# Optimization experiments

Measured on AMD Instinct MI355X. Metric: run time of the kernel, lower is better.

## Reference

```python
import jax, jax.numpy as jnp
import numpy as np

W, BHS, SEQ, H = 8, 2, 1024, 2048
FFN_PER = (4 * H) // W  # per-partition 4h width = 1024

def setup_inputs() -> dict:
    key = jax.random.key(0)
    k1, k2, k3 = jax.random.split(key, 3)
    # xavier-normal-ish scale for weights
    s1 = (2.0 / (H + FFN_PER)) ** 0.5
    s2 = (2.0 / (FFN_PER + H)) ** 0.5
    return {
        "hidden_states": jax.random.normal(k1, (W, BHS, SEQ, H), dtype=jnp.float32),
        "w1": jax.random.normal(k2, (W, H, FFN_PER), dtype=jnp.float32) * s1,
        "b1": jnp.zeros((W, 1, FFN_PER), dtype=jnp.float32),
        "w2": jax.random.normal(k3, (W, FFN_PER, H), dtype=jnp.float32) * s2,
        "b2": jnp.zeros((W, H), dtype=jnp.float32),
        "idx_list": jnp.arange(W, dtype=jnp.int64),
    }

def reference(hidden_states, w1, b1, w2, b2, idx_list):
    w, bhs, seq, h = hidden_states.shape
    # view [W, bhs, seq, h] -> [W, bhs*seq, h]
    x = hidden_states.reshape(w, bhs * seq, h)
    # column-parallel: baddbmm(bias, x, w1) -> [W, N, 4h/W]
    inter = jnp.einsum('wnh,whf->wnf', x, w1) + b1
    # exact (erf) gelu, matching torch F.gelu default
    inter = jax.nn.gelu(inter, approximate=False)
    # row-parallel: baddbmm(bias, inter, w2) -> [W, N, h]
    out_bias = b2[:, None, :]  # [W, 1, out]
    out = jnp.einsum('wnf,wfo->wno', inter, w2) + out_bias
    return (out, out_bias)
```

## Files before the change

kernel.cpp:

```cpp
#include <hip/hip_runtime.h>
#include <hip/hip_bf16.h>
#include <math.h>


typedef float f32x4 __attribute__((ext_vector_type(4)));
typedef short bf16x8 __attribute__((ext_vector_type(8)));
typedef short bf16x4 __attribute__((ext_vector_type(4)));
typedef unsigned short u16;

#define NW 8
#define MDIM 2048
#define HDIM 2048
#define FFN  1024

static __device__ __forceinline__ u16 f32_to_bf16_rn(float f) {
  union { float f; unsigned u; } v; v.f = f;
  unsigned r = v.u + 0x7FFF + ((v.u >> 16) & 1);
  return (u16)(r >> 16);
}

static __device__ __forceinline__ void gload_lds16(const void* g, void* l) {
  __builtin_amdgcn_global_load_lds(
      (const __attribute__((address_space(1))) void*)g,
      (__attribute__((address_space(3))) void*)l, 16, 0, 0);
}

__global__ void convert_bf16_kernel(const float* __restrict__ in,
                                    u16* __restrict__ out) {
  size_t i = (size_t)blockIdx.x * blockDim.x + threadIdx.x;
  f32x4 v = ((const f32x4*)in)[i];
  bf16x4 p;
  p[0] = (short)f32_to_bf16_rn(v.x);
  p[1] = (short)f32_to_bf16_rn(v.y);
  p[2] = (short)f32_to_bf16_rn(v.z);
  p[3] = (short)f32_to_bf16_rn(v.w);
  ((bf16x4*)out)[i] = p;
}

__global__ void convert_transpose_kernel(const float* __restrict__ in,
                                         u16* __restrict__ out, int R, int C) {
  __shared__ u16 tile[64][68];
  int w = blockIdx.z;
  int c0 = blockIdx.x * 64, r0 = blockIdx.y * 64;
  int t = threadIdx.x;
  const float* ip = in + (size_t)w * R * C;
  u16* op = out + (size_t)w * C * R;
  int tr = t >> 4;
  int tc4 = (t & 15) * 4;
#pragma unroll
  for (int j = 0; j < 4; ++j) {
    int r = tr + j * 16;
    f32x4 v = *(const f32x4*)(ip + (size_t)(r0 + r) * C + c0 + tc4);
    tile[r][tc4 + 0] = f32_to_bf16_rn(v.x);
    tile[r][tc4 + 1] = f32_to_bf16_rn(v.y);
    tile[r][tc4 + 2] = f32_to_bf16_rn(v.z);
    tile[r][tc4 + 3] = f32_to_bf16_rn(v.w);
  }
  __syncthreads();
#pragma unroll
  for (int j = 0; j < 4; ++j) {
    int c = tr + j * 16;
    bf16x4 p;
    p[0] = (short)tile[tc4 + 0][c];
    p[1] = (short)tile[tc4 + 1][c];
    p[2] = (short)tile[tc4 + 2][c];
    p[3] = (short)tile[tc4 + 3][c];
    *(bf16x4*)(op + (size_t)(c0 + c) * R + r0 + tc4) = p;
  }
}

#define STAGE_AH(dst, tt, h)                                                  \
  do {                                                                        \
    gload_lds16(gA + (size_t)(h) * 128 * rowK + (size_t)(tt) * 128,           \
                (dst) + (h) * 16384 + tid * 16);                              \
    gload_lds16(gA + ((size_t)(h) * 128 + 64) * rowK + (size_t)(tt) * 128,    \
                (dst) + (h) * 16384 + 8192 + tid * 16);                       \
  } while (0)
#define STAGE_BH(dst, tt, h)                                                  \
  do {                                                                        \
    gload_lds16(gB + (size_t)(h) * 128 * rowK + (size_t)(tt) * 128,           \
                (dst) + 32768 + (h) * 16384 + tid * 16);                      \
    gload_lds16(gB + ((size_t)(h) * 128 + 64) * rowK + (size_t)(tt) * 128,    \
                (dst) + 32768 + (h) * 16384 + 8192 + tid * 16);               \
  } while (0)

#define DO_PHASE(SB, q, first, STAGES, VMCODE)                                \
  {                                                                           \
    if (first) {                                                              \
      _Pragma("unroll") for (int jj = 0; jj < 4; ++jj)                        \
          _Pragma("unroll") for (int kk = 0; kk < 2; ++kk)                    \
              bfr[jj][kk] = *(const bf16x8*)((SB) + Boff +                    \
                  (brow + jj * 16 + ra) * 128 + (colsw ^ (kk << 6)));         \
    }                                                                         \
    _Pragma("unroll") for (int ii = 0; ii < 2; ++ii)                          \
        _Pragma("unroll") for (int kk = 0; kk < 2; ++kk)                      \
            afr[ii][kk] = *(const bf16x8*)((SB) + Aoff +                      \
                ((q)*32 + ii * 16 + ra) * 128 + (colsw ^ (kk << 6)));         \
    STAGES;                                                                   \
    __builtin_amdgcn_s_barrier();                                             \
    asm volatile("s_waitcnt lgkmcnt(0)" ::: "memory");                        \
    __builtin_amdgcn_sched_barrier(0);                                        \
    __builtin_amdgcn_s_setprio(1);                                            \
    _Pragma("unroll") for (int ii = 0; ii < 2; ++ii)                          \
        _Pragma("unroll") for (int jj = 0; jj < 4; ++jj)                      \
            _Pragma("unroll") for (int kk = 0; kk < 2; ++kk)                  \
                acc[(q)*2 + ii][jj] =                                         \
                    __builtin_amdgcn_mfma_f32_16x16x32_bf16(                  \
                        afr[ii][kk], bfr[jj][kk], acc[(q)*2 + ii][jj],        \
                        0, 0, 0);                                             \
    __builtin_amdgcn_s_setprio(0);                                            \
    VMCODE;                                                                   \
    __builtin_amdgcn_s_barrier();                                             \
  }

template <bool GELU, bool C_F32>
__global__ __launch_bounds__(512, 2) void mlp_gemm(
    const u16* __restrict__ A, const u16* __restrict__ Bt,
    const float* __restrict__ bias, void* __restrict__ Cptr,
    int M, int N, int K, int nN) {
  __shared__ __align__(16) char lds[131072];
  char* cur = lds;
  char* nxt = lds + 65536;

  const int bid = blockIdx.x;
  const int w = bid & 7;
  const int jb = bid >> 3;
  const int m0 = (jb / nN) * 256;
  const int n0 = (jb % nN) * 256;

  const int tid = threadIdx.x;
  const int wid = tid >> 6, lane = tid & 63;
  const int wr = wid >> 2, wc = wid & 3;
  const int qa = lane >> 4, ra = lane & 15;

  const u16* ap = A + (size_t)w * M * K;
  const u16* btp = Bt + (size_t)w * N * K;
  const float* bp = bias + (size_t)w * N;

  const size_t rowK = (size_t)K * 2;
  const int r8 = tid >> 3;
  const int csw = ((tid & 7) * 16) ^ ((r8 & 7) << 4);
  const char* gA = (const char*)ap + (size_t)(m0 + r8) * rowK + csw;
  const char* gB = (const char*)btp + (size_t)(n0 + r8) * rowK + csw;

  const int colsw = (qa * 16) ^ ((ra & 7) << 4);
  const int Aoff = wr * 16384;
  const int Boff = 32768 + (wc >> 1) * 16384;
  const int brow = (wc & 1) * 64;

  f32x4 acc[8][4];
#pragma unroll
  for (int i = 0; i < 8; ++i)
#pragma unroll
    for (int j = 0; j < 4; ++j)
#pragma unroll
      for (int r = 0; r < 4; ++r) acc[i][j][r] = 0.0f;

  const int NT = K >> 6;
  const int nIter = NT >> 1;

  STAGE_BH(cur, 0, 0); STAGE_BH(cur, 0, 1);
  STAGE_AH(cur, 0, 0); STAGE_AH(cur, 0, 1);
  STAGE_BH(nxt, 1, 0); STAGE_BH(nxt, 1, 1);
  asm volatile("s_waitcnt vmcnt(4)" ::: "memory");
  __builtin_amdgcn_sched_barrier(0);
  __builtin_amdgcn_s_barrier();

  bf16x8 bfr[4][2], afr[2][2];
  for (int it = 0; it < nIter; ++it) {
    const int t = it * 2;
    const bool s2 = (t + 2) < NT, s3 = (t + 3) < NT;

    DO_PHASE(cur, 0, 1, { STAGE_AH(nxt, t + 1, 0); }, {});
    DO_PHASE(cur, 1, 0,
             { STAGE_AH(nxt, t + 1, 1); if (s2) STAGE_BH(cur, t + 2, 0); }, {});
    DO_PHASE(cur, 2, 0, { if (s2) STAGE_BH(cur, t + 2, 1); }, {});
    DO_PHASE(cur, 3, 0, {}, {
      if (s2) asm volatile("s_waitcnt vmcnt(4)" ::: "memory");
      else    asm volatile("s_waitcnt vmcnt(0)" ::: "memory");
      __builtin_amdgcn_sched_barrier(0);
    });
    DO_PHASE(nxt, 0, 1, { if (s2) STAGE_AH(cur, t + 2, 0); }, {});
    DO_PHASE(nxt, 1, 0,
             { if (s2) STAGE_AH(cur, t + 2, 1); if (s3) STAGE_BH(nxt, t + 3, 0); }, {});
    DO_PHASE(nxt, 2, 0, { if (s3) STAGE_BH(nxt, t + 3, 1); }, {});
    DO_PHASE(nxt, 3, 0, {}, {
      if (s3) asm volatile("s_waitcnt vmcnt(4)" ::: "memory");
      else    asm volatile("s_waitcnt vmcnt(0)" ::: "memory");
      __builtin_amdgcn_sched_barrier(0);
    });
  }

#pragma unroll
  for (int i = 0; i < 8; ++i) {
#pragma unroll
    for (int j = 0; j < 4; ++j) {
      int col = n0 + wc * 64 + j * 16 + ra;
      float bv = bp[col];
#pragma unroll
      for (int r = 0; r < 4; ++r) {
        int row = m0 + wr * 128 + i * 16 + qa * 4 + r;
        float v = acc[i][j][r] + bv;
        if (GELU) v = 0.5f * v * (1.0f + erff(v * 0.70710678118654752f));
        if (C_F32)
          ((float*)Cptr)[(size_t)w * M * N + (size_t)row * N + col] = v;
        else
          ((u16*)Cptr)[(size_t)w * M * N + (size_t)row * N + col] =
              f32_to_bf16_rn(v);
      }
    }
  }
}

__global__ void bias_out_kernel(const float* __restrict__ b2,
                                float* __restrict__ outb) {
  int i = blockIdx.x * 256 + threadIdx.x;
  if (i < NW * HDIM) outb[i] = b2[i];
}

extern "C" void kernel_launch(void* const* d_in, const int* in_sizes, int n_in,
                              void* d_out, int out_size, void* d_ws,
                              size_t ws_size, hipStream_t stream) {
  const float* hs = (const float*)d_in[0];
  const float* w1 = (const float*)d_in[1];
  const float* b1 = (const float*)d_in[2];
  const float* w2 = (const float*)d_in[3];
  const float* b2 = (const float*)d_in[4];

  u16* W1t = (u16*)d_ws;
  u16* W2t = W1t + (size_t)NW * FFN * HDIM;
  u16* inter = W2t + (size_t)NW * HDIM * FFN;
  u16* XbWs = inter + (size_t)NW * MDIM * FFN;
  size_t need = ((size_t)NW * FFN * HDIM * 2 + (size_t)NW * MDIM * FFN +
                 (size_t)NW * MDIM * HDIM) * sizeof(u16);
  u16* Xb = (ws_size >= need) ? XbWs : (u16*)d_out;

  convert_bf16_kernel<<<dim3(NW * MDIM * HDIM / 4 / 256), 256, 0, stream>>>(hs, Xb);
  convert_transpose_kernel<<<dim3(FFN / 64, HDIM / 64, NW), 256, 0, stream>>>(
      w1, W1t, HDIM, FFN);
  convert_transpose_kernel<<<dim3(HDIM / 64, FFN / 64, NW), 256, 0, stream>>>(
      w2, W2t, FFN, HDIM);

  mlp_gemm<true, false><<<dim3(NW * (MDIM / 256) * (FFN / 256)), 512, 0, stream>>>(
      Xb, W1t, b1, inter, MDIM, FFN, HDIM, FFN / 256);
  mlp_gemm<false, true><<<dim3(NW * (MDIM / 256) * (HDIM / 256)), 512, 0, stream>>>(
      inter, W2t, b2, d_out, MDIM, HDIM, FFN, HDIM / 256);

  float* outb = (float*)d_out + (size_t)NW * MDIM * HDIM;
  bias_out_kernel<<<dim3((NW * HDIM + 255) / 256), 256, 0, stream>>>(b2, outb);
}
```

Measured before the change: 245.1 us.

## Fuse fp32-to-bf16 activation conversion into first GEMM's A-tile loads

```diff
diff --git a/kernel.cpp b/kernel.cpp
--- a/kernel.cpp
+++ b/kernel.cpp
@@ -23,18 +23,6 @@
   __builtin_amdgcn_global_load_lds(
       (const __attribute__((address_space(1))) void*)g,
       (__attribute__((address_space(3))) void*)l, 16, 0, 0);
-}
-
-__global__ void convert_bf16_kernel(const float* __restrict__ in,
-                                    u16* __restrict__ out) {
-  size_t i = (size_t)blockIdx.x * blockDim.x + threadIdx.x;
-  f32x4 v = ((const f32x4*)in)[i];
-  bf16x4 p;
-  p[0] = (short)f32_to_bf16_rn(v.x);
-  p[1] = (short)f32_to_bf16_rn(v.y);
-  p[2] = (short)f32_to_bf16_rn(v.z);
-  p[3] = (short)f32_to_bf16_rn(v.w);
-  ((bf16x4*)out)[i] = p;
 }
 
 __global__ void convert_transpose_kernel(const float* __restrict__ in,
@@ -83,6 +71,24 @@
     gload_lds16(gB + ((size_t)(h) * 128 + 64) * rowK + (size_t)(tt) * 128,    \
                 (dst) + 32768 + (h) * 16384 + 8192 + tid * 16);               \
   } while (0)
+
+#define A_LOADS(tt)                                                           \
+  _Pragma("unroll") for (int h_ = 0; h_ < 2; ++h_)                            \
+  _Pragma("unroll") for (int g_ = 0; g_ < 2; ++g_)                            \
+  _Pragma("unroll") for (int j_ = 0; j_ < 2; ++j_)                            \
+      ar[h_][g_][j_] = *(const f32x4*)(gAf +                                  \
+          (size_t)(h_ * 128 + g_ * 64) * rowKf + (size_t)(tt) * 256 + j_ * 16)
+
+#define A_WRITES(dst)                                                         \
+  _Pragma("unroll") for (int h_ = 0; h_ < 2; ++h_)                            \
+  _Pragma("unroll") for (int g_ = 0; g_ < 2; ++g_) {                          \
+    bf16x8 p_;                                                                \
+    _Pragma("unroll") for (int e_ = 0; e_ < 4; ++e_) {                        \
+      p_[e_]     = (short)f32_to_bf16_rn(ar[h_][g_][0][e_]);                  \
+      p_[e_ + 4] = (short)f32_to_bf16_rn(ar[h_][g_][1][e_]);                  \
+    }                                                                         \
+    *(bf16x8*)((dst) + h_ * 16384 + g_ * 8192 + tid * 16) = p_;               \
+  }
 
 #define DO_PHASE(SB, q, first, STAGES, VMCODE)                                \
   {                                                                           \
@@ -113,9 +119,9 @@
     __builtin_amdgcn_s_barrier();                                             \
   }
 
-template <bool GELU, bool C_F32>
+template <bool A_F32, bool GELU, bool C_F32>
 __global__ __launch_bounds__(512, 2) void mlp_gemm(
-    const u16* __restrict__ A, const u16* __restrict__ Bt,
+    const void* __restrict__ Aptr, const u16* __restrict__ Bt,
     const float* __restrict__ bias, void* __restrict__ Cptr,
     int M, int N, int K, int nN) {
   __shared__ __align__(16) char lds[131072];
@@ -133,14 +139,17 @@
   const int wr = wid >> 2, wc = wid & 3;
   const int qa = lane >> 4, ra = lane & 15;
 
-  const u16* ap = A + (size_t)w * M * K;
   const u16* btp = Bt + (size_t)w * N * K;
   const float* bp = bias + (size_t)w * N;
 
   const size_t rowK = (size_t)K * 2;
+  const size_t rowKf = (size_t)K * 4;
   const int r8 = tid >> 3;
   const int csw = ((tid & 7) * 16) ^ ((r8 & 7) << 4);
-  const char* gA = (const char*)ap + (size_t)(m0 + r8) * rowK + csw;
+  const char* gA = (const char*)((const u16*)Aptr + (size_t)w * M * K) +
+                   (size_t)(m0 + r8) * rowK + csw;
+  const char* gAf = (const char*)((const float*)Aptr + (size_t)w * M * K) +
+                    (size_t)(m0 + r8) * rowKf + 2 * csw;
   const char* gB = (const char*)btp + (size_t)(n0 + r8) * rowK + csw;
 
   const int colsw = (qa * 16) ^ ((ra & 7) << 4);
@@ -159,36 +168,72 @@
   const int NT = K >> 6;
   const int nIter = NT >> 1;
 
-  STAGE_BH(cur, 0, 0); STAGE_BH(cur, 0, 1);
-  STAGE_AH(cur, 0, 0); STAGE_AH(cur, 0, 1);
-  STAGE_BH(nxt, 1, 0); STAGE_BH(nxt, 1, 1);
-  asm volatile("s_waitcnt vmcnt(4)" ::: "memory");
-  __builtin_amdgcn_sched_barrier(0);
-  __builtin_amdgcn_s_barrier();
-
   bf16x8 bfr[4][2], afr[2][2];
-  for (int it = 0; it < nIter; ++it) {
-    const int t = it * 2;
-    const bool s2 = (t + 2) < NT, s3 = (t + 3) < NT;
-
-    DO_PHASE(cur, 0, 1, { STAGE_AH(nxt, t + 1, 0); }, {});
-    DO_PHASE(cur, 1, 0,
-             { STAGE_AH(nxt, t + 1, 1); if (s2) STAGE_BH(cur, t + 2, 0); }, {});
-    DO_PHASE(cur, 2, 0, { if (s2) STAGE_BH(cur, t + 2, 1); }, {});
-    DO_PHASE(cur, 3, 0, {}, {
-      if (s2) asm volatile("s_waitcnt vmcnt(4)" ::: "memory");
-      else    asm volatile("s_waitcnt vmcnt(0)" ::: "memory");
-      __builtin_amdgcn_sched_barrier(0);
-    });
-    DO_PHASE(nxt, 0, 1, { if (s2) STAGE_AH(cur, t + 2, 0); }, {});
-    DO_PHASE(nxt, 1, 0,
-             { if (s2) STAGE_AH(cur, t + 2, 1); if (s3) STAGE_BH(nxt, t + 3, 0); }, {});
-    DO_PHASE(nxt, 2, 0, { if (s3) STAGE_BH(nxt, t + 3, 1); }, {});
-    DO_PHASE(nxt, 3, 0, {}, {
-      if (s3) asm volatile("s_waitcnt vmcnt(4)" ::: "memory");
-      else    asm volatile("s_waitcnt vmcnt(0)" ::: "memory");
-      __builtin_amdgcn_sched_barrier(0);
-    });
+  f32x4 ar[2][2][2];
+
+  if (A_F32) {
+    A_LOADS(0);
+    STAGE_BH(cur, 0, 0); STAGE_BH(cur, 0, 1);
+    STAGE_BH(nxt, 1, 0); STAGE_BH(nxt, 1, 1);
+    asm volatile("s_waitcnt vmcnt(4)" ::: "memory");
+    A_WRITES(cur);
+    asm volatile("s_waitcnt lgkmcnt(0)" ::: "memory");
+    __builtin_amdgcn_sched_barrier(0);
+    __builtin_amdgcn_s_barrier();
+
+    for (int it = 0; it < nIter; ++it) {
+      const int t = it * 2;
+      const bool s2 = (t + 2) < NT;
+
+      DO_PHASE(cur, 0, 1, { A_LOADS(t + 1); }, {});
+      DO_PHASE(cur, 1, 0, { if (s2) STAGE_BH(cur, t + 2, 0); }, {});
+      DO_PHASE(cur, 2, 0, { if (s2) STAGE_BH(cur, t + 2, 1); }, {});
+      DO_PHASE(cur, 3, 0, {
+        if (s2) asm volatile("s_waitcnt vmcnt(4)" ::: "memory");
+        else    asm volatile("s_waitcnt vmcnt(0)" ::: "memory");
+        A_WRITES(nxt);
+      }, {});
+      DO_PHASE(nxt, 0, 1, { if (s2) A_LOADS(t + 2); }, {});
+      DO_PHASE(nxt, 1, 0, { if (s2) STAGE_BH(nxt, t + 3, 0); }, {});
+      DO_PHASE(nxt, 2, 0, { if (s2) STAGE_BH(nxt, t + 3, 1); }, {});
+      DO_PHASE(nxt, 3, 0, {
+        if (s2) {
+          asm volatile("s_waitcnt vmcnt(4)" ::: "memory");
+          A_WRITES(cur);
+        }
+      }, {});
+    }
+  } else {
+    STAGE_BH(cur, 0, 0); STAGE_BH(cur, 0, 1);
+    STAGE_AH(cur, 0, 0); STAGE_AH(cur, 0, 1);
+    STAGE_BH(nxt, 1, 0); STAGE_BH(nxt, 1, 1);
+    asm volatile("s_waitcnt vmcnt(4)" ::: "memory");
+    __builtin_amdgcn_sched_barrier(0);
+    __builtin_amdgcn_s_barrier();
+
+    for (int it = 0; it < nIter; ++it) {
+      const int t = it * 2;
+      const bool s2 = (t + 2) < NT, s3 = (t + 3) < NT;
+
+      DO_PHASE(cur, 0, 1, { STAGE_AH(nxt, t + 1, 0); }, {});
+      DO_PHASE(cur, 1, 0,
+               { STAGE_AH(nxt, t + 1, 1); if (s2) STAGE_BH(cur, t + 2, 0); }, {});
+      DO_PHASE(cur, 2, 0, { if (s2) STAGE_BH(cur, t + 2, 1); }, {});
+      DO_PHASE(cur, 3, 0, {}, {
+        if (s2) asm volatile("s_waitcnt vmcnt(4)" ::: "memory");
+        else    asm volatile("s_waitcnt vmcnt(0)" ::: "memory");
+        __builtin_amdgcn_sched_barrier(0);
+      });
+      DO_PHASE(nxt, 0, 1, { if (s2) STAGE_AH(cur, t + 2, 0); }, {});
+      DO_PHASE(nxt, 1, 0,
+               { if (s2) STAGE_AH(cur, t + 2, 1); if (s3) STAGE_BH(nxt, t + 3, 0); }, {});
+      DO_PHASE(nxt, 2, 0, { if (s3) STAGE_BH(nxt, t + 3, 1); }, {});
+      DO_PHASE(nxt, 3, 0, {}, {
+        if (s3) asm volatile("s_waitcnt vmcnt(4)" ::: "memory");
+        else    asm volatile("s_waitcnt vmcnt(0)" ::: "memory");
+        __builtin_amdgcn_sched_barrier(0);
+      });
+    }
   }
 
 #pragma unroll
@@ -230,21 +275,18 @@
   u16* W1t = (u16*)d_ws;
   u16* W2t = W1t + (size_t)NW * FFN * HDIM;
   u16* inter = W2t + (size_t)NW * HDIM * FFN;
-  u16* XbWs = inter + (size_t)NW * MDIM * FFN;
-  size_t need = ((size_t)NW * FFN * HDIM * 2 + (size_t)NW * MDIM * FFN +
-                 (size_t)NW * MDIM * HDIM) * sizeof(u16);
-  u16* Xb = (ws_size >= need) ? XbWs : (u16*)d_out;
-
-  convert_bf16_kernel<<<dim3(NW * MDIM * HDIM / 4 / 256), 256, 0, stream>>>(hs, Xb);
+
   convert_transpose_kernel<<<dim3(FFN / 64, HDIM / 64, NW), 256, 0, stream>>>(
       w1, W1t, HDIM, FFN);
   convert_transpose_kernel<<<dim3(HDIM / 64, FFN / 64, NW), 256, 0, stream>>>(
       w2, W2t, FFN, HDIM);
 
-  mlp_gemm<true, false><<<dim3(NW * (MDIM / 256) * (FFN / 256)), 512, 0, stream>>>(
-      Xb, W1t, b1, inter, MDIM, FFN, HDIM, FFN / 256);
-  mlp_gemm<false, true><<<dim3(NW * (MDIM / 256) * (HDIM / 256)), 512, 0, stream>>>(
-      inter, W2t, b2, d_out, MDIM, HDIM, FFN, HDIM / 256);
+  mlp_gemm<true, true, false>
+      <<<dim3(NW * (MDIM / 256) * (FFN / 256)), 512, 0, stream>>>(
+          hs, W1t, b1, inter, MDIM, FFN, HDIM, FFN / 256);
+  mlp_gemm<false, false, true>
+      <<<dim3(NW * (MDIM / 256) * (HDIM / 256)), 512, 0, stream>>>(
+          inter, W2t, b2, d_out, MDIM, HDIM, FFN, HDIM / 256);
 
   float* outb = (float*)d_out + (size_t)NW * MDIM * HDIM;
   bias_out_kernel<<<dim3((NW * HDIM + 255) / 256), 256, 0, stream>>>(b2, outb);
```

New measurement: 247.2 us. No clear change (+0.8%).

## Double-buffer LDS-to-register fragments in GEMM and fold bias copy into convert

Applied to the files above, without the earlier changes.

```diff
diff --git a/kernel.cpp b/kernel.cpp
--- a/kernel.cpp
+++ b/kernel.cpp
@@ -26,8 +26,16 @@
 }
 
 __global__ void convert_bf16_kernel(const float* __restrict__ in,
-                                    u16* __restrict__ out) {
-  size_t i = (size_t)blockIdx.x * blockDim.x + threadIdx.x;
+                                    u16* __restrict__ out,
+                                    const float* __restrict__ b2,
+                                    float* __restrict__ outb) {
+  int bid = blockIdx.x;
+  if (bid >= NW * MDIM * HDIM / 4 / 256) {
+    int i = (bid - NW * MDIM * HDIM / 4 / 256) * 256 + threadIdx.x;
+    if (i < NW * HDIM) outb[i] = b2[i];
+    return;
+  }
+  size_t i = (size_t)bid * blockDim.x + threadIdx.x;
   f32x4 v = ((const f32x4*)in)[i];
   bf16x4 p;
   p[0] = (short)f32_to_bf16_rn(v.x);
@@ -84,18 +92,19 @@
                 (dst) + 32768 + (h) * 16384 + 8192 + tid * 16);               \
   } while (0)
 
-#define DO_PHASE(SB, q, first, STAGES, VMCODE)                                \
+#define LOAD_A(DST, SB, q)                                                    \
+  _Pragma("unroll") for (int ii = 0; ii < 2; ++ii)                            \
+      _Pragma("unroll") for (int kk = 0; kk < 2; ++kk)                        \
+          DST[ii][kk] = *(const bf16x8*)((SB) + Aoff +                        \
+              ((q)*32 + ii * 16 + ra) * 128 + (colsw ^ (kk << 6)))
+#define LOAD_B(DST, SB)                                                       \
+  _Pragma("unroll") for (int jj = 0; jj < 4; ++jj)                            \
+      _Pragma("unroll") for (int kk = 0; kk < 2; ++kk)                        \
+          DST[jj][kk] = *(const bf16x8*)((SB) + Boff +                        \
+              (brow + jj * 16 + ra) * 128 + (colsw ^ (kk << 6)))
+
+#define DO_PHASE(q, AF, BF, STAGES, VMCODE, PREFETCH)                         \
   {                                                                           \
-    if (first) {                                                              \
-      _Pragma("unroll") for (int jj = 0; jj < 4; ++jj)                        \
-          _Pragma("unroll") for (int kk = 0; kk < 2; ++kk)                    \
-              bfr[jj][kk] = *(const bf16x8*)((SB) + Boff +                    \
-                  (brow + jj * 16 + ra) * 128 + (colsw ^ (kk << 6)));         \
-    }                                                                         \
-    _Pragma("unroll") for (int ii = 0; ii < 2; ++ii)                          \
-        _Pragma("unroll") for (int kk = 0; kk < 2; ++kk)                      \
-            afr[ii][kk] = *(const bf16x8*)((SB) + Aoff +                      \
-                ((q)*32 + ii * 16 + ra) * 128 + (colsw ^ (kk << 6)));         \
     STAGES;                                                                   \
     __builtin_amdgcn_s_barrier();                                             \
     asm volatile("s_waitcnt lgkmcnt(0)" ::: "memory");                        \
@@ -106,10 +115,12 @@
             _Pragma("unroll") for (int kk = 0; kk < 2; ++kk)                  \
                 acc[(q)*2 + ii][jj] =                                         \
                     __builtin_amdgcn_mfma_f32_16x16x32_bf16(                  \
-                        afr[ii][kk], bfr[jj][kk], acc[(q)*2 + ii][jj],        \
+                        AF[ii][kk], BF[jj][kk], acc[(q)*2 + ii][jj],          \
                         0, 0, 0);                                             \
     __builtin_amdgcn_s_setprio(0);                                            \
     VMCODE;                                                                   \
+    PREFETCH;                                                                 \
+    __builtin_amdgcn_sched_barrier(0);                                        \
     __builtin_amdgcn_s_barrier();                                             \
   }
 
@@ -166,29 +177,40 @@
   __builtin_amdgcn_sched_barrier(0);
   __builtin_amdgcn_s_barrier();
 
-  bf16x8 bfr[4][2], afr[2][2];
+  bf16x8 afrA[2][2], afrB[2][2], bfrA[4][2], bfrB[4][2];
+  LOAD_B(bfrA, cur);
+  LOAD_A(afrA, cur, 0);
+  __builtin_amdgcn_sched_barrier(0);
+
   for (int it = 0; it < nIter; ++it) {
     const int t = it * 2;
-    const bool s2 = (t + 2) < NT, s3 = (t + 3) < NT;
-
-    DO_PHASE(cur, 0, 1, { STAGE_AH(nxt, t + 1, 0); }, {});
-    DO_PHASE(cur, 1, 0,
-             { STAGE_AH(nxt, t + 1, 1); if (s2) STAGE_BH(cur, t + 2, 0); }, {});
-    DO_PHASE(cur, 2, 0, { if (s2) STAGE_BH(cur, t + 2, 1); }, {});
-    DO_PHASE(cur, 3, 0, {}, {
+    const bool s2 = (t + 2) < NT;
+
+    DO_PHASE(0, afrA, bfrA, { STAGE_AH(nxt, t + 1, 0); }, {},
+             { LOAD_A(afrB, cur, 1); });
+    DO_PHASE(1, afrB, bfrA,
+             { STAGE_AH(nxt, t + 1, 1); if (s2) STAGE_BH(cur, t + 2, 0); }, {},
+             { LOAD_A(afrA, cur, 2); });
+    DO_PHASE(2, afrA, bfrA, { if (s2) STAGE_BH(cur, t + 2, 1); }, {},
+             { LOAD_A(afrB, cur, 3); });
+    DO_PHASE(3, afrB, bfrA, {}, {
       if (s2) asm volatile("s_waitcnt vmcnt(4)" ::: "memory");
       else    asm volatile("s_waitcnt vmcnt(0)" ::: "memory");
       __builtin_amdgcn_sched_barrier(0);
-    });
-    DO_PHASE(nxt, 0, 1, { if (s2) STAGE_AH(cur, t + 2, 0); }, {});
-    DO_PHASE(nxt, 1, 0,
-             { if (s2) STAGE_AH(cur, t + 2, 1); if (s3) STAGE_BH(nxt, t + 3, 0); }, {});
-    DO_PHASE(nxt, 2, 0, { if (s3) STAGE_BH(nxt, t + 3, 1); }, {});
-    DO_PHASE(nxt, 3, 0, {}, {
-      if (s3) asm volatile("s_waitcnt vmcnt(4)" ::: "memory");
+    }, { LOAD_B(bfrB, nxt); LOAD_A(afrA, nxt, 0); });
+
+    DO_PHASE(0, afrA, bfrB, { if (s2) STAGE_AH(cur, t + 2, 0); }, {},
+             { LOAD_A(afrB, nxt, 1); });
+    DO_PHASE(1, afrB, bfrB,
+             { if (s2) STAGE_AH(cur, t + 2, 1); if (s2) STAGE_BH(nxt, t + 3, 0); }, {},
+             { LOAD_A(afrA, nxt, 2); });
+    DO_PHASE(2, afrA, bfrB, { if (s2) STAGE_BH(nxt, t + 3, 1); }, {},
+             { LOAD_A(afrB, nxt, 3); });
+    DO_PHASE(3, afrB, bfrB, {}, {
+      if (s2) asm volatile("s_waitcnt vmcnt(4)" ::: "memory");
       else    asm volatile("s_waitcnt vmcnt(0)" ::: "memory");
       __builtin_amdgcn_sched_barrier(0);
-    });
+    }, { LOAD_B(bfrA, cur); LOAD_A(afrA, cur, 0); });
   }
 
 #pragma unroll
@@ -212,12 +234,6 @@
   }
 }
 
-__global__ void bias_out_kernel(const float* __restrict__ b2,
-                                float* __restrict__ outb) {
-  int i = blockIdx.x * 256 + threadIdx.x;
-  if (i < NW * HDIM) outb[i] = b2[i];
-}
-
 extern "C" void kernel_launch(void* const* d_in, const int* in_sizes, int n_in,
                               void* d_out, int out_size, void* d_ws,
                               size_t ws_size, hipStream_t stream) {
@@ -235,17 +251,19 @@
                  (size_t)NW * MDIM * HDIM) * sizeof(u16);
   u16* Xb = (ws_size >= need) ? XbWs : (u16*)d_out;
 
-  convert_bf16_kernel<<<dim3(NW * MDIM * HDIM / 4 / 256), 256, 0, stream>>>(hs, Xb);
+  float* outb = (float*)d_out + (size_t)NW * MDIM * HDIM;
+
+  convert_bf16_kernel<<<dim3(NW * MDIM * HDIM / 4 / 256 + 16), 256, 0,
+                        stream>>>(hs, Xb, b2, outb);
   convert_transpose_kernel<<<dim3(FFN / 64, HDIM / 64, NW), 256, 0, stream>>>(
       w1, W1t, HDIM, FFN);
   convert_transpose_kernel<<<dim3(HDIM / 64, FFN / 64, NW), 256, 0, stream>>>(
       w2, W2t, FFN, HDIM);
 
-  mlp_gemm<true, false><<<dim3(NW * (MDIM / 256) * (FFN / 256)), 512, 0, stream>>>(
-      Xb, W1t, b1, inter, MDIM, FFN, HDIM, FFN / 256);
-  mlp_gemm<false, true><<<dim3(NW * (MDIM / 256) * (HDIM / 256)), 512, 0, stream>>>(
-      inter, W2t, b2, d_out, MDIM, HDIM, FFN, HDIM / 256);
-
-  float* outb = (float*)d_out + (size_t)NW * MDIM * HDIM;
-  bias_out_kernel<<<dim3((NW * HDIM + 255) / 256), 256, 0, stream>>>(b2, outb);
-}
+  mlp_gemm<true, false>
+      <<<dim3(NW * (MDIM / 256) * (FFN / 256)), 512, 0, stream>>>(
+          Xb, W1t, b1, inter, MDIM, FFN, HDIM, FFN / 256);
+  mlp_gemm<false, true>
+      <<<dim3(NW * (MDIM / 256) * (HDIM / 256)), 512, 0, stream>>>(
+          inter, W2t, b2, d_out, MDIM, HDIM, FFN, HDIM / 256);
+}
```

Measured after the change: 231.6 us. -5.5%, faster.
